# Kernel tuning notes

Hardware: AMD Instinct MI355X
Metric: run time of the kernel (lower is better)

Reference implementation:

```python
import jax, jax.numpy as jnp
import numpy as np

ALPHA, GAMMA, EPS = 0.25, 2.0, 1e-8
COST_CLASS, COST_BBOX, COST_GIOU = 2.0, 5.0, 2.0


def box_cxcywh_to_xyxy(b):
    cx, cy, w, h = jnp.split(b, 4, axis=-1)
    return jnp.concatenate([cx - 0.5 * w, cy - 0.5 * h, cx + 0.5 * w, cy + 0.5 * h], axis=-1)


def setup_inputs() -> dict:
    key = jax.random.key(0)
    k1, k2, k3, k4 = jax.random.split(key, 4)
    bs, Q, C, T = 16, 900, 80, 1600
    return {
        "pred_logits": jax.random.normal(k1, (bs, Q, C), jnp.float32),
        "pred_boxes": jax.random.uniform(k2, (bs, Q, 4), jnp.float32),
        "tgt_labels": jax.random.randint(k3, (T,), 0, C),
        "tgt_boxes": jax.random.uniform(k4, (T, 4), jnp.float32),
        "g_size": 3,
    }


def reference(pred_logits, pred_boxes, tgt_labels, tgt_boxes, g_size):
    bs, Q, _ = pred_logits.shape
    # focal classification cost (use_focal=True path)
    p = jax.nn.sigmoid(pred_logits.reshape(bs * Q, -1))  # [N, C]
    neg = (1.0 - ALPHA) * p ** GAMMA * (-jnp.log(1.0 - p + EPS))
    pos = ALPHA * (1.0 - p) ** GAMMA * (-jnp.log(p + EPS))
    cost_class = (pos - neg)[:, tgt_labels]  # [N, T]
    # L1 box cost (cdist p=1)
    out_bbox = pred_boxes.reshape(bs * Q, 4)
    cost_bbox = jnp.abs(out_bbox[:, None, :] - tgt_bbox_b(tgt_boxes)).sum(-1)  # [N, T]
    # GIoU cost
    b1 = box_cxcywh_to_xyxy(out_bbox)  # [N, 4]
    b2 = box_cxcywh_to_xyxy(tgt_boxes)  # [T, 4]
    area1 = (b1[:, 2] - b1[:, 0]) * (b1[:, 3] - b1[:, 1])
    area2 = (b2[:, 2] - b2[:, 0]) * (b2[:, 3] - b2[:, 1])
    lt = jnp.maximum(b1[:, None, :2], b2[None, :, :2])
    rb = jnp.minimum(b1[:, None, 2:], b2[None, :, 2:])
    wh = jnp.clip(rb - lt, 0.0)
    inter = wh[..., 0] * wh[..., 1]
    union = area1[:, None] + area2[None, :] - inter
    iou = inter / union
    elt = jnp.minimum(b1[:, None, :2], b2[None, :, :2])
    erb = jnp.maximum(b1[:, None, 2:], b2[None, :, 2:])
    ewh = jnp.clip(erb - elt, 0.0)
    earea = ewh[..., 0] * ewh[..., 1]
    giou = iou - (earea - union) / earea
    # weighted total cost, then group reduction (note: original names it Cmin but takes max over the group dim)
    Cmat = COST_BBOX * cost_bbox + COST_CLASS * cost_class + COST_GIOU * (-giou)
    Cmin = Cmat.reshape(bs, Q // g_size, g_size, -1).max(axis=2)  # [bs, Q//g, T]
    return Cmin


def tgt_bbox_b(tgt_boxes):
    return tgt_boxes[None, :, :]
```

## Files before the change

kernel.cpp:

```cpp
#include <hip/hip_runtime.h>

#define ALPHA 0.25f
#define EPS   1e-8f

constexpr int BS     = 16;
constexpr int QN     = 900;
constexpr int CN     = 80;
constexpr int GS     = 3;
constexpr int WAVES  = 2;
constexpr int NT     = WAVES * 64;
constexpr int ROWS   = WAVES * GS;
constexpr int TBATCH = 5;

__global__ __launch_bounds__(NT) void fused_cost_kernel(
    const float* __restrict__ pred_logits,
    const float* __restrict__ pred_boxes,
    const int*   __restrict__ tgt_labels,
    const float* __restrict__ tgt_boxes,
    float*       __restrict__ out,
    int T)
{
    __shared__ float s_cc[ROWS * CN];

    const int tid  = threadIdx.x;
    const int wv   = tid >> 6;
    const int lane = tid & 63;
    const int b    = blockIdx.y;
    const int n0   = b * QN + blockIdx.x * ROWS;

    const float* lg0 = pred_logits + (size_t)n0 * CN;
    for (int k = tid; k < ROWS * CN; k += NT) {
        float x = lg0[k];
        float p = __fdividef(1.0f, 1.0f + __expf(-x));
        float omp = 1.0f - p;
        float pos = ALPHA * omp * omp * (-__logf(p + EPS));
        float neg = (1.0f - ALPHA) * p * p * (-__logf(omp + EPS));
        s_cc[k] = 2.0f * (pos - neg) + 2.0f;
    }

    float Pcx[GS], Pcy[GS], Pw[GS], Ph[GS];
    float Px0[GS], Py0[GS], Px1[GS], Py1[GS], Pa[GS];
    #pragma unroll
    for (int g = 0; g < GS; ++g) {
        const float4 pb = ((const float4*)pred_boxes)[n0 + wv * GS + g];
        Pcx[g] = pb.x;  Pcy[g] = pb.y;  Pw[g] = pb.z;  Ph[g] = pb.w;
        Px0[g] = pb.x - 0.5f * pb.z;  Py0[g] = pb.y - 0.5f * pb.w;
        Px1[g] = pb.x + 0.5f * pb.z;  Py1[g] = pb.y + 0.5f * pb.w;
        Pa[g]  = pb.z * pb.w;
    }
    __syncthreads();

    const int qg = blockIdx.x * WAVES + wv;
    float* __restrict__ outp = out + (size_t)(b * (QN / GS) + qg) * T;
    const int ccRow = (wv * GS) * CN;

    const int nPass = T / (64 * TBATCH);

    for (int p = 0; p < nPass; ++p) {
        float4 tr[TBATCH];
        int    lab[TBATCH];
        int    tIdx[TBATCH];
        #pragma unroll
        for (int j = 0; j < TBATCH; ++j) {
            tIdx[j] = (p * TBATCH + j) * 64 + lane;
            tr[j]   = ((const float4*)tgt_boxes)[tIdx[j]];
            lab[j]  = tgt_labels[tIdx[j]];
        }
        float ccs[TBATCH][GS];
        #pragma unroll
        for (int j = 0; j < TBATCH; ++j)
            #pragma unroll
            for (int g = 0; g < GS; ++g)
                ccs[j][g] = s_cc[ccRow + g * CN + lab[j]];

        #pragma unroll
        for (int j = 0; j < TBATCH; ++j) {
            const float tcx = tr[j].x, tcy = tr[j].y, tw = tr[j].z, th = tr[j].w;
            const float tx0 = tcx - 0.5f * tw, ty0 = tcy - 0.5f * th;
            const float tx1 = tcx + 0.5f * tw, ty1 = tcy + 0.5f * th;
            const float ta  = tw * th;

            float m = -3.402823466e+38f;
            #pragma unroll
            for (int g = 0; g < GS; ++g) {
                float l1 = fabsf(Pcx[g] - tcx) + fabsf(Pcy[g] - tcy)
                         + fabsf(Pw[g]  - tw)  + fabsf(Ph[g]  - th);

                float iw = fminf(Px1[g], tx1) - fmaxf(Px0[g], tx0);
                float ih = fminf(Py1[g], ty1) - fmaxf(Py0[g], ty0);
                float inter = fmaxf(iw, 0.0f) * fmaxf(ih, 0.0f);
                float uni   = Pa[g] + ta - inter;

                float ew = fmaxf(Px1[g], tx1) - fminf(Px0[g], tx0);
                float eh = fmaxf(Py1[g], ty1) - fminf(Py0[g], ty0);
                float earea = ew * eh;

                float num = fmaf(inter, earea, uni * uni);
                float q   = __fdividef(num, uni * earea);

                float cost = fmaf(5.0f, l1, fmaf(-2.0f, q, ccs[j][g]));
                m = fmaxf(m, cost);
            }
            outp[tIdx[j]] = m;
        }
    }
}

extern "C" void kernel_launch(void* const* d_in, const int* in_sizes, int n_in,
                              void* d_out, int out_size, void* d_ws, size_t ws_size,
                              hipStream_t stream) {
    const float* pred_logits = (const float*)d_in[0];
    const float* pred_boxes  = (const float*)d_in[1];
    const int*   tgt_labels  = (const int*)d_in[2];
    const float* tgt_boxes   = (const float*)d_in[3];

    const int T = in_sizes[2];
    float* out = (float*)d_out;

    dim3 grid((QN / GS) / WAVES, BS);
    fused_cost_kernel<<<grid, NT, 0, stream>>>(
        pred_logits, pred_boxes, tgt_labels, tgt_boxes, out, T);
}
```

Measured before the change: 106.9 us.

## Process two query groups per wave and split targets across grid z

Each wave now computes two query groups (6 prediction rows) per target, so each target box and label load is reused across more rows. The target dimension is split into 5 chunks across blockIdx.z, which raises the number of blocks for better occupancy. The enclosing-box width and height are derived algebraically from the intersection extents instead of separate min/max ops. The cost is that the focal-class table is recomputed in every z-slice, five times per row block, and each thread holds more register state.

```diff
diff --git a/kernel.cpp b/kernel.cpp
--- a/kernel.cpp
+++ b/kernel.cpp
@@ -8,9 +8,11 @@
 constexpr int CN     = 80;
 constexpr int GS     = 3;
 constexpr int WAVES  = 2;
+constexpr int QG_PER_WAVE = 2;
+constexpr int RPW    = QG_PER_WAVE * GS;
+constexpr int ROWS   = WAVES * RPW;
 constexpr int NT     = WAVES * 64;
-constexpr int ROWS   = WAVES * GS;
-constexpr int TBATCH = 5;
+constexpr int TSPLIT = 5;
 
 __global__ __launch_bounds__(NT) void fused_cost_kernel(
     const float* __restrict__ pred_logits,
@@ -38,11 +40,12 @@
         s_cc[k] = 2.0f * (pos - neg) + 2.0f;
     }
 
-    float Pcx[GS], Pcy[GS], Pw[GS], Ph[GS];
-    float Px0[GS], Py0[GS], Px1[GS], Py1[GS], Pa[GS];
+    const int r0 = wv * RPW;
+    float Pcx[RPW], Pcy[RPW], Pw[RPW], Ph[RPW];
+    float Px0[RPW], Py0[RPW], Px1[RPW], Py1[RPW], Pa[RPW];
     #pragma unroll
-    for (int g = 0; g < GS; ++g) {
-        const float4 pb = ((const float4*)pred_boxes)[n0 + wv * GS + g];
+    for (int g = 0; g < RPW; ++g) {
+        const float4 pb = ((const float4*)pred_boxes)[n0 + r0 + g];
         Pcx[g] = pb.x;  Pcy[g] = pb.y;  Pw[g] = pb.z;  Ph[g] = pb.w;
         Px0[g] = pb.x - 0.5f * pb.z;  Py0[g] = pb.y - 0.5f * pb.w;
         Px1[g] = pb.x + 0.5f * pb.z;  Py1[g] = pb.y + 0.5f * pb.w;
@@ -50,59 +53,53 @@
     }
     __syncthreads();
 
-    const int qg = blockIdx.x * WAVES + wv;
-    float* __restrict__ outp = out + (size_t)(b * (QN / GS) + qg) * T;
-    const int ccRow = (wv * GS) * CN;
+    const int qgA = blockIdx.x * (WAVES * QG_PER_WAVE) + wv * QG_PER_WAVE;
+    float* __restrict__ outA = out + (size_t)(b * (QN / GS) + qgA) * T;
+    float* __restrict__ outB = outA + T;
+    const int ccRow = r0 * CN;
 
-    const int nPass = T / (64 * TBATCH);
+    const int tChunk = T / TSPLIT;
+    const int t0     = blockIdx.z * tChunk + lane;
 
-    for (int p = 0; p < nPass; ++p) {
-        float4 tr[TBATCH];
-        int    lab[TBATCH];
-        int    tIdx[TBATCH];
+    #pragma unroll
+    for (int i = 0; i < tChunk / 64; ++i) {
+        const int t = t0 + (i << 6);
+        const float4 tr = ((const float4*)tgt_boxes)[t];
+        const int lab   = tgt_labels[t];
+
+        const float tcx = tr.x, tcy = tr.y, tw = tr.z, th = tr.w;
+        const float tx0 = tcx - 0.5f * tw, ty0 = tcy - 0.5f * th;
+        const float tx1 = tcx + 0.5f * tw, ty1 = tcy + 0.5f * th;
+        const float ta  = tw * th;
+
+        float ccs[RPW];
         #pragma unroll
-        for (int j = 0; j < TBATCH; ++j) {
-            tIdx[j] = (p * TBATCH + j) * 64 + lane;
-            tr[j]   = ((const float4*)tgt_boxes)[tIdx[j]];
-            lab[j]  = tgt_labels[tIdx[j]];
+        for (int g = 0; g < RPW; ++g) ccs[g] = s_cc[ccRow + g * CN + lab];
+
+        float mA = -3.402823466e+38f, mB = -3.402823466e+38f;
+        #pragma unroll
+        for (int g = 0; g < RPW; ++g) {
+            float l1 = fabsf(Pcx[g] - tcx) + fabsf(Pcy[g] - tcy)
+                     + fabsf(Pw[g]  - tw)  + fabsf(Ph[g]  - th);
+
+            float iw = fminf(Px1[g], tx1) - fmaxf(Px0[g], tx0);
+            float ih = fminf(Py1[g], ty1) - fmaxf(Py0[g], ty0);
+            float inter = fmaxf(iw, 0.0f) * fmaxf(ih, 0.0f);
+            float uni   = Pa[g] + ta - inter;
+
+            float ew = Pw[g] + tw - iw;
+            float eh = Ph[g] + th - ih;
+            float earea = ew * eh;
+
+            float num = fmaf(inter, earea, uni * uni);
+            float q   = __fdividef(num, uni * earea);
+
+            float cost = fmaf(5.0f, l1, fmaf(-2.0f, q, ccs[g]));
+            if (g < GS) mA = fmaxf(mA, cost);
+            else        mB = fmaxf(mB, cost);
         }
-        float ccs[TBATCH][GS];
-        #pragma unroll
-        for (int j = 0; j < TBATCH; ++j)
-            #pragma unroll
-            for (int g = 0; g < GS; ++g)
-                ccs[j][g] = s_cc[ccRow + g * CN + lab[j]];
-
-        #pragma unroll
-        for (int j = 0; j < TBATCH; ++j) {
-            const float tcx = tr[j].x, tcy = tr[j].y, tw = tr[j].z, th = tr[j].w;
-            const float tx0 = tcx - 0.5f * tw, ty0 = tcy - 0.5f * th;
-            const float tx1 = tcx + 0.5f * tw, ty1 = tcy + 0.5f * th;
-            const float ta  = tw * th;
-
-            float m = -3.402823466e+38f;
-            #pragma unroll
-            for (int g = 0; g < GS; ++g) {
-                float l1 = fabsf(Pcx[g] - tcx) + fabsf(Pcy[g] - tcy)
-                         + fabsf(Pw[g]  - tw)  + fabsf(Ph[g]  - th);
-
-                float iw = fminf(Px1[g], tx1) - fmaxf(Px0[g], tx0);
-                float ih = fminf(Py1[g], ty1) - fmaxf(Py0[g], ty0);
-                float inter = fmaxf(iw, 0.0f) * fmaxf(ih, 0.0f);
-                float uni   = Pa[g] + ta - inter;
-
-                float ew = fmaxf(Px1[g], tx1) - fminf(Px0[g], tx0);
-                float eh = fmaxf(Py1[g], ty1) - fminf(Py0[g], ty0);
-                float earea = ew * eh;
-
-                float num = fmaf(inter, earea, uni * uni);
-                float q   = __fdividef(num, uni * earea);
-
-                float cost = fmaf(5.0f, l1, fmaf(-2.0f, q, ccs[j][g]));
-                m = fmaxf(m, cost);
-            }
-            outp[tIdx[j]] = m;
-        }
+        outA[t] = mA;
+        outB[t] = mB;
     }
 }
 
@@ -117,7 +114,7 @@
     const int T = in_sizes[2];
     float* out = (float*)d_out;
 
-    dim3 grid((QN / GS) / WAVES, BS);
+    dim3 grid((QN / GS) / (WAVES * QG_PER_WAVE), BS, TSPLIT);
     fused_cost_kernel<<<grid, NT, 0, stream>>>(
         pred_logits, pred_boxes, tgt_labels, tgt_boxes, out, T);
 }
```

Result: slower. 115.8 us (+8.3%).
